# Kernel tuning notes

Hardware: AMD Instinct MI355X
Metric: run time of the kernel (lower is better)

Reference implementation:

```python
import math
import jax, jax.numpy as jnp
import numpy as np

B, S, H, NH = 2, 1536, 2048, 16
DH = H // NH  # 128
FP16_MIN = float(jnp.finfo(jnp.float16).min)


def setup_inputs() -> dict:
    key = jax.random.key(0)
    ks = jax.random.split(key, 6)
    std = 0.02
    return {
        "x": jax.random.normal(ks[0], (B, S, H), dtype=jnp.float32),
        "attention_bias": jax.random.normal(ks[1], (B, NH, S, S), dtype=jnp.float32),
        "Wq": jax.random.normal(ks[2], (H, H), dtype=jnp.float32) * std,
        "Wk": jax.random.normal(ks[3], (H, H), dtype=jnp.float32) * std,
        "Wv": jax.random.normal(ks[4], (H, H), dtype=jnp.float32) * std,
        "Wo": jax.random.normal(ks[5], (H, H), dtype=jnp.float32) * std,
    }


def reference(x, attention_bias, Wq, Wk, Wv, Wo):
    b, s, h = x.shape
    # QKV projections (nn.Linear with bias=False: y = x @ W.T)
    q = (x @ Wq.T).reshape(b, s, NH, DH).transpose(0, 2, 1, 3)  # b h s d
    k = (x @ Wk.T).reshape(b, s, NH, DH).transpose(0, 2, 1, 3)
    v = (x @ Wv.T).reshape(b, s, NH, DH).transpose(0, 2, 1, 3)
    # bias[:, :, -s:, -s:] is identity here since bias is already [b,h,s,s]
    bias = attention_bias[:, :, -s:, -s:]
    # mask where tril(bias) == 0 (upper triangle and any exact zeros in lower)
    masked = jnp.tril(bias) == 0
    bias = jnp.where(masked, FP16_MIN, bias)
    # torch SDPA default scale = 1/sqrt(head_dim) (module's softmax_scale unused)
    scale = 1.0 / math.sqrt(DH)
    scores = jnp.einsum("bhqd,bhkd->bhqk", q, k) * scale + bias
    attn = jax.nn.softmax(scores, axis=-1)
    out = jnp.einsum("bhqk,bhkd->bhqd", attn, v)  # b h s d
    out = out.transpose(0, 2, 1, 3).reshape(b, s, h)  # b s (h d)
    return out @ Wo.T
```

## Files before the change

### kernel.cpp

```cpp
#include <hip/hip_runtime.h>
#include <cstdint>
#include <stddef.h>

typedef short short8 __attribute__((ext_vector_type(8)));
typedef float floatx4 __attribute__((ext_vector_type(4)));
typedef unsigned short ushortx4 __attribute__((ext_vector_type(4)));

#define MFMA16(a, b, c) __builtin_amdgcn_mfma_f32_16x16x32_bf16((a), (b), (c), 0, 0, 0)

static constexpr int Bv = 2, Sv = 1536, Hv = 2048, NHv = 16, DHv = 128;
static constexpr int Mv = Bv * Sv;
static constexpr float SCALE = 0.08838834764831845f;

__device__ inline unsigned short f2bf(float f) {
  union { float f; unsigned u; } c; c.f = f;
  unsigned u = c.u;
  u += 0x7fffu + ((u >> 16) & 1u);
  return (unsigned short)(u >> 16);
}

__device__ inline void async_copy16(const void* g, void* l) {
  auto gp = reinterpret_cast<__attribute__((address_space(1))) uint32_t*>(
      reinterpret_cast<uintptr_t>(g));
  auto lp = reinterpret_cast<__attribute__((address_space(3))) uint32_t*>(
      reinterpret_cast<uintptr_t>(l));
  __builtin_amdgcn_global_load_lds(gp, lp, 16, 0, 0);
}

__global__ void cvt_all_kernel(const float* __restrict__ x,
    const float* __restrict__ Wq, const float* __restrict__ Wk,
    const float* __restrict__ Wv, const float* __restrict__ Wo,
    unsigned short* __restrict__ xb, unsigned short* __restrict__ wqb,
    unsigned short* __restrict__ wkb, unsigned short* __restrict__ wvb,
    unsigned short* __restrict__ wob) {
  const int i = blockIdx.x * 256 + threadIdx.x;
  const int nx4 = (Mv * Hv) / 4;
  const float* src; unsigned short* dst; int j; float scl = 1.0f;
  if (i < nx4) {
    src = x; dst = xb; j = i;
  } else {
    const int i2 = i - nx4;
    const int wsel = i2 >> 20;
    j = i2 & ((1 << 20) - 1);
    if (wsel == 0)      { src = Wq; dst = wqb; scl = SCALE; }
    else if (wsel == 1) { src = Wk; dst = wkb; }
    else if (wsel == 2) { src = Wv; dst = wvb; }
    else                { src = Wo; dst = wob; }
  }
  const float4 v = reinterpret_cast<const float4*>(src)[j];
  ushortx4 o;
  o[0] = f2bf(v.x * scl); o[1] = f2bf(v.y * scl);
  o[2] = f2bf(v.z * scl); o[3] = f2bf(v.w * scl);
  reinterpret_cast<ushortx4*>(dst)[j] = o;
}

__global__ __launch_bounds__(256, 2) void qkv_fused_kernel(
    const unsigned short* __restrict__ A,
    const unsigned short* __restrict__ Wq, const unsigned short* __restrict__ Wk,
    const unsigned short* __restrict__ Wv,
    unsigned short* __restrict__ Cq, unsigned short* __restrict__ Ck,
    unsigned short* __restrict__ Cv) {
  __shared__ __align__(16) unsigned short As[128 * 64];
  __shared__ __align__(16) unsigned short Bs[3][128 * 64];
  const int tid = threadIdx.x;
  const int w = tid >> 6, lane = tid & 63;
  const int quad = lane >> 4, l15 = lane & 15;
  const int wr = w >> 1, wc = w & 1;
  const int tileM = blockIdx.y * 128, tileN = blockIdx.x * 128;

  floatx4 aq[4][4], ak[4][4], av[4][4];
#pragma unroll
  for (int i = 0; i < 4; ++i)
#pragma unroll
    for (int j = 0; j < 4; ++j)
#pragma unroll
      for (int r = 0; r < 4; ++r) { aq[i][j][r] = 0.0f; ak[i][j][r] = 0.0f; av[i][j][r] = 0.0f; }

  size_t aoff[4], boff[4]; int lbs[4];
#pragma unroll
  for (int m = 0; m < 4; ++m) {
    const int slot = m * 256 + tid;
    const int row = slot >> 3, blk = slot & 7;
    const int sw = (blk ^ (row & 7)) * 8;
    aoff[m] = (size_t)(tileM + row) * 2048 + sw;
    boff[m] = (size_t)(tileN + row) * 2048 + sw;
    lbs[m] = (m * 256 + w * 64) * 8;
  }

  for (int k0 = 0; k0 < 2048; k0 += 64) {
    __syncthreads();
#pragma unroll
    for (int m = 0; m < 4; ++m) async_copy16(A + aoff[m] + k0, As + lbs[m]);
#pragma unroll
    for (int m = 0; m < 4; ++m) async_copy16(Wq + boff[m] + k0, Bs[0] + lbs[m]);
#pragma unroll
    for (int m = 0; m < 4; ++m) async_copy16(Wk + boff[m] + k0, Bs[1] + lbs[m]);
#pragma unroll
    for (int m = 0; m < 4; ++m) async_copy16(Wv + boff[m] + k0, Bs[2] + lbs[m]);
    __syncthreads();
#pragma unroll
    for (int kk = 0; kk < 2; ++kk) {
      const int swz = (((kk * 4 + quad) ^ (l15 & 7)) * 8);
      short8 af[4];
#pragma unroll
      for (int i = 0; i < 4; ++i)
        af[i] = *(const short8*)(As + (wr * 64 + i * 16 + l15) * 64 + swz);
      {
        short8 bq[4];
#pragma unroll
        for (int j = 0; j < 4; ++j)
          bq[j] = *(const short8*)(Bs[0] + (wc * 64 + j * 16 + l15) * 64 + swz);
#pragma unroll
        for (int i = 0; i < 4; ++i)
#pragma unroll
          for (int j = 0; j < 4; ++j) aq[i][j] = MFMA16(af[i], bq[j], aq[i][j]);
      }
      {
        short8 bk[4];
#pragma unroll
        for (int j = 0; j < 4; ++j)
          bk[j] = *(const short8*)(Bs[1] + (wc * 64 + j * 16 + l15) * 64 + swz);
#pragma unroll
        for (int i = 0; i < 4; ++i)
#pragma unroll
          for (int j = 0; j < 4; ++j) ak[i][j] = MFMA16(af[i], bk[j], ak[i][j]);
      }
      {
        short8 bv[4];
#pragma unroll
        for (int j = 0; j < 4; ++j)
          bv[j] = *(const short8*)(Bs[2] + (wc * 64 + j * 16 + l15) * 64 + swz);
#pragma unroll
        for (int i = 0; i < 4; ++i)
#pragma unroll
          for (int j = 0; j < 4; ++j) av[i][j] = MFMA16(af[i], bv[j], av[i][j]);
      }
    }
  }

#pragma unroll
  for (int i = 0; i < 4; ++i) {
#pragma unroll
    for (int r = 0; r < 4; ++r) {
      const size_t row = tileM + wr * 64 + i * 16 + quad * 4 + r;
#pragma unroll
      for (int j = 0; j < 4; ++j) {
        const int col = tileN + wc * 64 + j * 16 + l15;
        Cq[row * 2048 + col] = f2bf(aq[i][j][r]);
        Ck[row * 2048 + col] = f2bf(ak[i][j][r]);
        Cv[row * 2048 + col] = f2bf(av[i][j][r]);
      }
    }
  }
}

template <int TM, bool WF32>
__global__ __launch_bounds__(256) void gemm_bt_kernel(
    const unsigned short* __restrict__ A,
    const unsigned short* __restrict__ W0,
    void* __restrict__ C0) {
  constexpr int MI = TM / 32;
  __shared__ __align__(16) unsigned short As[2][TM * 64];
  __shared__ __align__(16) unsigned short Bs[2][128 * 64];
  const unsigned short* W = W0;
  const int tid = threadIdx.x;
  const int w = tid >> 6, lane = tid & 63;
  const int quad = lane >> 4, l15 = lane & 15;
  const int wr = w >> 1, wc = w & 1;
  const int tileM = blockIdx.y * TM, tileN = blockIdx.x * 128;

  floatx4 acc[MI][4];
#pragma unroll
  for (int i = 0; i < MI; ++i)
#pragma unroll
    for (int j = 0; j < 4; ++j)
#pragma unroll
      for (int r = 0; r < 4; ++r) acc[i][j][r] = 0.0f;

  size_t aoff[MI]; int alb[MI];
#pragma unroll
  for (int m = 0; m < MI; ++m) {
    const int slot = m * 256 + tid;
    const int row = slot >> 3, blk = slot & 7;
    aoff[m] = (size_t)(tileM + row) * 2048 + ((blk ^ (row & 7)) * 8);
    alb[m] = (m * 256 + w * 64) * 8;
  }
  size_t boff[4]; int blb[4];
#pragma unroll
  for (int m = 0; m < 4; ++m) {
    const int slot = m * 256 + tid;
    const int row = slot >> 3, blk = slot & 7;
    boff[m] = (size_t)(tileN + row) * 2048 + ((blk ^ (row & 7)) * 8);
    blb[m] = (m * 256 + w * 64) * 8;
  }

#pragma unroll
  for (int m = 0; m < MI; ++m) async_copy16(A + aoff[m], As[0] + alb[m]);
#pragma unroll
  for (int m = 0; m < 4; ++m) async_copy16(W + boff[m], Bs[0] + blb[m]);
  __syncthreads();

  for (int t = 0; t < 32; ++t) {
    const int cur = t & 1;
    if (t < 31) {
      const int kn = (t + 1) * 64;
#pragma unroll
      for (int m = 0; m < MI; ++m)
        async_copy16(A + aoff[m] + kn, As[cur ^ 1] + alb[m]);
#pragma unroll
      for (int m = 0; m < 4; ++m)
        async_copy16(W + boff[m] + kn, Bs[cur ^ 1] + blb[m]);
    }
    const unsigned short* as_ = As[cur];
    const unsigned short* bs_ = Bs[cur];
#pragma unroll
    for (int kk = 0; kk < 2; ++kk) {
      const int swz = (((kk * 4 + quad) ^ (l15 & 7)) * 8);
      short8 af[MI], bfr[4];
#pragma unroll
      for (int i = 0; i < MI; ++i)
        af[i] = *(const short8*)(as_ + (wr * (TM / 2) + i * 16 + l15) * 64 + swz);
#pragma unroll
      for (int j = 0; j < 4; ++j)
        bfr[j] = *(const short8*)(bs_ + (wc * 64 + j * 16 + l15) * 64 + swz);
#pragma unroll
      for (int i = 0; i < MI; ++i)
#pragma unroll
        for (int j = 0; j < 4; ++j) acc[i][j] = MFMA16(af[i], bfr[j], acc[i][j]);
    }
    __syncthreads();
  }

  void* C = C0;
#pragma unroll
  for (int i = 0; i < MI; ++i) {
#pragma unroll
    for (int r = 0; r < 4; ++r) {
      const int row = tileM + wr * (TM / 2) + i * 16 + quad * 4 + r;
#pragma unroll
      for (int j = 0; j < 4; ++j) {
        const int col = tileN + wc * 64 + j * 16 + l15;
        if (WF32)
          ((float*)C)[(size_t)row * 2048 + col] = acc[i][j][r];
        else
          ((unsigned short*)C)[(size_t)row * 2048 + col] = f2bf(acc[i][j][r]);
      }
    }
  }
}

__global__ __launch_bounds__(256) void vtrans_kernel(
    const unsigned short* __restrict__ V, unsigned short* __restrict__ Vtg) {
  __shared__ unsigned short Vs[64 * 132];
  const int t0 = blockIdx.x * 64, h = blockIdx.y, b = blockIdx.z;
  const int tid = threadIdx.x;
  const int w = tid >> 6, lane = tid & 63;
#pragma unroll
  for (int m = 0; m < 4; ++m) {
    const int idx = m * 256 + tid;
    const int tr = idx >> 4, blk = idx & 15;
    const unsigned short* src = V + ((size_t)(b * Sv) + t0 + tr) * Hv + h * DHv + blk * 8;
    ushortx4 v0 = *(const ushortx4*)(src);
    ushortx4 v1 = *(const ushortx4*)(src + 4);
    *(ushortx4*)(Vs + tr * 132 + blk * 8) = v0;
    *(ushortx4*)(Vs + tr * 132 + blk * 8 + 4) = v1;
  }
  __syncthreads();
  const size_t obase = ((size_t)(b * NHv + h) * DHv) * Sv + t0;
#pragma unroll 4
  for (int p = 0; p < 32; ++p) {
    const int d = p * 4 + w;
    Vtg[obase + (size_t)d * Sv + lane] = Vs[lane * 132 + d];
  }
}

__global__ __launch_bounds__(256) void attn_kernel(
    const unsigned short* __restrict__ Qg, const unsigned short* __restrict__ Kg,
    const unsigned short* __restrict__ Vtg, const float* __restrict__ bias,
    unsigned short* __restrict__ Og) {
  __shared__ __align__(16) unsigned short Ks[2][64 * 128];
  __shared__ __align__(16) unsigned short Vt[2][128 * 64];
  __shared__ __align__(16) unsigned short Ps[4 * 16 * 64];

  const int xb = blockIdx.x;
  const int qt = (xb & 1) ? (23 - (xb >> 1)) : (xb >> 1);
  const int h = blockIdx.y, b = blockIdx.z;
  const int q0 = qt * 64;
  const int tid = threadIdx.x;
  const int w = tid >> 6, lane = tid & 63;
  const int quad = lane >> 4, l15 = lane & 15;

  const size_t bh_base = (size_t)(b * Sv) * Hv + (size_t)h * DHv;
  const size_t vt_base = ((size_t)(b * NHv + h) * DHv) * Sv;

  short8 qf[4];
  {
    const unsigned short* qbase = Qg + bh_base + (size_t)(q0 + w * 16 + l15) * Hv;
#pragma unroll
    for (int kk = 0; kk < 4; ++kk)
      qf[kk] = *(const short8*)(qbase + kk * 32 + quad * 8);
  }

  floatx4 o[8];
#pragma unroll
  for (int n = 0; n < 8; ++n)
#pragma unroll
    for (int r = 0; r < 4; ++r) o[n][r] = 0.0f;
  float lrow[4] = {0.0f, 0.0f, 0.0f, 0.0f};

  const float* biasbase = bias + (size_t)(b * NHv + h) * Sv * Sv;
  unsigned short* pw = Ps + w * 1024;

  size_t koff[4], voff[4]; int lbs[4];
#pragma unroll
  for (int m = 0; m < 4; ++m) {
    const int sK = m * 256 + tid;
    const int rK = sK >> 4, bK = sK & 15;
    koff[m] = bh_base + (size_t)rK * Hv + ((bK ^ (rK & 15)) * 8);
    const int sV = m * 256 + tid;
    const int rV = sV >> 3, bV = sV & 7;
    voff[m] = vt_base + (size_t)rV * Sv + ((bV ^ (rV & 7)) * 8);
    lbs[m] = (m * 256 + w * 64) * 8;
  }

  float bv[4][4];
#pragma unroll
  for (int r = 0; r < 4; ++r) {
    const size_t brow = (size_t)(q0 + w * 16 + quad * 4 + r) * Sv;
#pragma unroll
    for (int j = 0; j < 4; ++j) bv[r][j] = biasbase[brow + j * 16 + l15];
  }

#pragma unroll
  for (int m = 0; m < 4; ++m) {
    async_copy16(Kg + koff[m], Ks[0] + lbs[m]);
    async_copy16(Vtg + voff[m], Vt[0] + lbs[m]);
  }
  __syncthreads();

  for (int kt = 0; kt <= qt; ++kt) {
    const int k0 = kt * 64;
    const int cur = kt & 1;

    if (kt < qt) {
      const int k1 = k0 + 64;
#pragma unroll
      for (int m = 0; m < 4; ++m) {
        async_copy16(Kg + koff[m] + (size_t)k1 * Hv, Ks[cur ^ 1] + lbs[m]);
        async_copy16(Vtg + voff[m] + k1, Vt[cur ^ 1] + lbs[m]);
      }
    }

    const int kn = (kt < qt) ? k0 + 64 : k0;
    float bvn[4][4];
#pragma unroll
    for (int r = 0; r < 4; ++r) {
      const size_t brow = (size_t)(q0 + w * 16 + quad * 4 + r) * Sv;
#pragma unroll
      for (int j = 0; j < 4; ++j) bvn[r][j] = biasbase[brow + kn + j * 16 + l15];
    }

    const unsigned short* ks_ = Ks[cur];
    const unsigned short* vt_ = Vt[cur];
    floatx4 sacc[4];
    __builtin_amdgcn_s_setprio(1);
#pragma unroll
    for (int j = 0; j < 4; ++j) {
#pragma unroll
      for (int r = 0; r < 4; ++r) sacc[j][r] = 0.0f;
      const int kr = j * 16 + l15;
#pragma unroll
      for (int kk = 0; kk < 4; ++kk) {
        const int g = kk * 4 + quad;
        short8 bfrag = *(const short8*)(ks_ + kr * 128 + (g ^ (kr & 15)) * 8);
        sacc[j] = MFMA16(qf[kk], bfrag, sacc[j]);
      }
    }
    __builtin_amdgcn_s_setprio(0);

    const bool diag = (kt == qt);
#pragma unroll
    for (int r = 0; r < 4; ++r) {
      const int qrow = q0 + w * 16 + quad * 4 + r;
      const int prow = quad * 4 + r;
      float acc_l = 0.0f;
#pragma unroll
      for (int j = 0; j < 4; ++j) {
        const int col = j * 16 + l15;
        float p = __expf(sacc[j][r] + bv[r][j]);
        if (diag && (k0 + col) > qrow) p = 0.0f;
        acc_l += p;
        pw[prow * 64 + ((col >> 3) ^ (prow & 7)) * 8 + (col & 7)] = f2bf(p);
      }
      lrow[r] += acc_l;
    }
#pragma unroll
    for (int r = 0; r < 4; ++r)
#pragma unroll
      for (int j = 0; j < 4; ++j) bv[r][j] = bvn[r][j];

    __builtin_amdgcn_s_setprio(1);
#pragma unroll
    for (int kk = 0; kk < 2; ++kk) {
      const int g = kk * 4 + quad;
      short8 pa = *(const short8*)(pw + l15 * 64 + (g ^ (l15 & 7)) * 8);
#pragma unroll
      for (int n = 0; n < 8; ++n) {
        const int dr = n * 16 + l15;
        short8 vbf = *(const short8*)(vt_ + dr * 64 + (g ^ (dr & 7)) * 8);
        o[n] = MFMA16(pa, vbf, o[n]);
      }
    }
    __builtin_amdgcn_s_setprio(0);

    __syncthreads();
  }

#pragma unroll
  for (int r = 0; r < 4; ++r) {
    float ls = lrow[r];
#pragma unroll
    for (int off = 1; off < 16; off <<= 1) ls += __shfl_xor(ls, off, 64);
    const float inv = 1.0f / ls;
    const int qrow = q0 + w * 16 + quad * 4 + r;
    const size_t rowbase = bh_base + (size_t)qrow * Hv;
#pragma unroll
    for (int n = 0; n < 8; ++n)
      Og[rowbase + n * 16 + l15] = f2bf(o[n][r] * inv);
  }
}

extern "C" void kernel_launch(void* const* d_in, const int* in_sizes, int n_in,
                              void* d_out, int out_size, void* d_ws, size_t ws_size,
                              hipStream_t stream) {
  const float* x = (const float*)d_in[0];
  const float* bias = (const float*)d_in[1];
  const float* Wq = (const float*)d_in[2];
  const float* Wk = (const float*)d_in[3];
  const float* Wv = (const float*)d_in[4];
  const float* Wo = (const float*)d_in[5];
  float* out = (float*)d_out;

  unsigned short* xb = (unsigned short*)d_ws;
  unsigned short* wqb = xb + (size_t)Mv * Hv;
  unsigned short* wkb = wqb + (size_t)Hv * Hv;
  unsigned short* wvb = wkb + (size_t)Hv * Hv;
  unsigned short* wob = wvb + (size_t)Hv * Hv;
  unsigned short* qb = wob + (size_t)Hv * Hv;
  unsigned short* kb = qb + (size_t)Mv * Hv;
  unsigned short* vb = kb + (size_t)Mv * Hv;
  unsigned short* ob = vb + (size_t)Mv * Hv;
  unsigned short* vtb = xb;
  const size_t needed = ((size_t)Mv * Hv * 5 + (size_t)Hv * Hv * 4) * 2;
  if (ws_size < needed) return;

  const int cvt_n = (Mv * Hv) / 4 + Hv * Hv;
  cvt_all_kernel<<<dim3(cvt_n / 256), 256, 0, stream>>>(
      x, Wq, Wk, Wv, Wo, xb, wqb, wkb, wvb, wob);

  qkv_fused_kernel<<<dim3(16, 24), 256, 0, stream>>>(
      xb, wqb, wkb, wvb, qb, kb, vb);

  vtrans_kernel<<<dim3(24, 16, 2), 256, 0, stream>>>(vb, vtb);

  attn_kernel<<<dim3(24, NHv, Bv), 256, 0, stream>>>(qb, kb, vtb, bias, ob);

  gemm_bt_kernel<128, true><<<dim3(16, 24), 256, 0, stream>>>(ob, wob, out);
}
```

Measured before the change: 613.2 us.

## Process two 64-row query tiles per attention block to reuse K/V tiles

Each attention workgroup now handles 128 query rows, split into two 64-row groups. Both groups share each staged K/V tile in LDS, which halves K/V global traffic, and the grid shrinks from 24 to 12 query blocks. Launch bounds are set to request two blocks per CU. The cost is doubled accumulator registers and fewer blocks (384), which may lower occupancy and load balance across CUs.

```diff
diff --git a/kernel.cpp b/kernel.cpp
--- a/kernel.cpp
+++ b/kernel.cpp
@@ -274,7 +274,7 @@
   }
 }
 
-__global__ __launch_bounds__(256) void attn_kernel(
+__global__ __launch_bounds__(256, 2) void attn_kernel(
     const unsigned short* __restrict__ Qg, const unsigned short* __restrict__ Kg,
     const unsigned short* __restrict__ Vtg, const float* __restrict__ bias,
     unsigned short* __restrict__ Og) {
@@ -283,9 +283,9 @@
   __shared__ __align__(16) unsigned short Ps[4 * 16 * 64];
 
   const int xb = blockIdx.x;
-  const int qt = (xb & 1) ? (23 - (xb >> 1)) : (xb >> 1);
+  const int qt = (xb & 1) ? (11 - (xb >> 1)) : (xb >> 1);
   const int h = blockIdx.y, b = blockIdx.z;
-  const int q0 = qt * 64;
+  const int q0 = qt * 128;
   const int tid = threadIdx.x;
   const int w = tid >> 6, lane = tid & 63;
   const int quad = lane >> 4, l15 = lane & 15;
@@ -293,20 +293,24 @@
   const size_t bh_base = (size_t)(b * Sv) * Hv + (size_t)h * DHv;
   const size_t vt_base = ((size_t)(b * NHv + h) * DHv) * Sv;
 
-  short8 qf[4];
-  {
-    const unsigned short* qbase = Qg + bh_base + (size_t)(q0 + w * 16 + l15) * Hv;
+  short8 qf[2][4];
+#pragma unroll
+  for (int g = 0; g < 2; ++g) {
+    const unsigned short* qbase =
+        Qg + bh_base + (size_t)(q0 + g * 64 + w * 16 + l15) * Hv;
 #pragma unroll
     for (int kk = 0; kk < 4; ++kk)
-      qf[kk] = *(const short8*)(qbase + kk * 32 + quad * 8);
-  }
-
-  floatx4 o[8];
-#pragma unroll
-  for (int n = 0; n < 8; ++n)
-#pragma unroll
-    for (int r = 0; r < 4; ++r) o[n][r] = 0.0f;
-  float lrow[4] = {0.0f, 0.0f, 0.0f, 0.0f};
+      qf[g][kk] = *(const short8*)(qbase + kk * 32 + quad * 8);
+  }
+
+  floatx4 o[2][8];
+#pragma unroll
+  for (int g = 0; g < 2; ++g)
+#pragma unroll
+    for (int n = 0; n < 8; ++n)
+#pragma unroll
+      for (int r = 0; r < 4; ++r) o[g][n][r] = 0.0f;
+  float lrow[2][4] = {{0.0f, 0.0f, 0.0f, 0.0f}, {0.0f, 0.0f, 0.0f, 0.0f}};
 
   const float* biasbase = bias + (size_t)(b * NHv + h) * Sv * Sv;
   unsigned short* pw = Ps + w * 1024;
@@ -323,12 +327,12 @@
     lbs[m] = (m * 256 + w * 64) * 8;
   }
 
-  float bv[4][4];
+  float bv0n[4][4];
 #pragma unroll
   for (int r = 0; r < 4; ++r) {
     const size_t brow = (size_t)(q0 + w * 16 + quad * 4 + r) * Sv;
 #pragma unroll
-    for (int j = 0; j < 4; ++j) bv[r][j] = biasbase[brow + j * 16 + l15];
+    for (int j = 0; j < 4; ++j) bv0n[r][j] = biasbase[brow + j * 16 + l15];
   }
 
 #pragma unroll
@@ -338,11 +342,12 @@
   }
   __syncthreads();
 
-  for (int kt = 0; kt <= qt; ++kt) {
+  const int nkt = 2 * qt + 2;
+  for (int kt = 0; kt < nkt; ++kt) {
     const int k0 = kt * 64;
     const int cur = kt & 1;
 
-    if (kt < qt) {
+    if (kt + 1 < nkt) {
       const int k1 = k0 + 64;
 #pragma unroll
       for (int m = 0; m < 4; ++m) {
@@ -351,82 +356,98 @@
       }
     }
 
-    const int kn = (kt < qt) ? k0 + 64 : k0;
-    float bvn[4][4];
+    float bv[2][4][4];
+#pragma unroll
+    for (int r = 0; r < 4; ++r)
+#pragma unroll
+      for (int j = 0; j < 4; ++j) bv[0][r][j] = bv0n[r][j];
+#pragma unroll
+    for (int r = 0; r < 4; ++r) {
+      const size_t brow = (size_t)(q0 + 64 + w * 16 + quad * 4 + r) * Sv;
+#pragma unroll
+      for (int j = 0; j < 4; ++j) bv[1][r][j] = biasbase[brow + k0 + j * 16 + l15];
+    }
+    const int knext = (kt + 1 < nkt) ? k0 + 64 : k0;
 #pragma unroll
     for (int r = 0; r < 4; ++r) {
       const size_t brow = (size_t)(q0 + w * 16 + quad * 4 + r) * Sv;
 #pragma unroll
-      for (int j = 0; j < 4; ++j) bvn[r][j] = biasbase[brow + kn + j * 16 + l15];
+      for (int j = 0; j < 4; ++j) bv0n[r][j] = biasbase[brow + knext + j * 16 + l15];
     }
 
     const unsigned short* ks_ = Ks[cur];
     const unsigned short* vt_ = Vt[cur];
-    floatx4 sacc[4];
-    __builtin_amdgcn_s_setprio(1);
-#pragma unroll
-    for (int j = 0; j < 4; ++j) {
-#pragma unroll
-      for (int r = 0; r < 4; ++r) sacc[j][r] = 0.0f;
-      const int kr = j * 16 + l15;
-#pragma unroll
-      for (int kk = 0; kk < 4; ++kk) {
-        const int g = kk * 4 + quad;
-        short8 bfrag = *(const short8*)(ks_ + kr * 128 + (g ^ (kr & 15)) * 8);
-        sacc[j] = MFMA16(qf[kk], bfrag, sacc[j]);
-      }
-    }
-    __builtin_amdgcn_s_setprio(0);
-
-    const bool diag = (kt == qt);
+
+#pragma unroll
+    for (int g = 0; g < 2; ++g) {
+      const int rbase = q0 + g * 64;
+      if (k0 == rbase + 64) continue;
+      const bool diag = (k0 == rbase);
+
+      floatx4 sacc[4];
+      __builtin_amdgcn_s_setprio(1);
+#pragma unroll
+      for (int j = 0; j < 4; ++j) {
+#pragma unroll
+        for (int r = 0; r < 4; ++r) sacc[j][r] = 0.0f;
+        const int kr = j * 16 + l15;
+#pragma unroll
+        for (int kk = 0; kk < 4; ++kk) {
+          const int gq = kk * 4 + quad;
+          short8 bfrag = *(const short8*)(ks_ + kr * 128 + (gq ^ (kr & 15)) * 8);
+          sacc[j] = MFMA16(qf[g][kk], bfrag, sacc[j]);
+        }
+      }
+      __builtin_amdgcn_s_setprio(0);
+
+#pragma unroll
+      for (int r = 0; r < 4; ++r) {
+        const int qrow = rbase + w * 16 + quad * 4 + r;
+        const int prow = quad * 4 + r;
+        float acc_l = 0.0f;
+#pragma unroll
+        for (int j = 0; j < 4; ++j) {
+          const int col = j * 16 + l15;
+          float p = __expf(sacc[j][r] + bv[g][r][j]);
+          if (diag && (k0 + col) > qrow) p = 0.0f;
+          acc_l += p;
+          pw[prow * 64 + ((col >> 3) ^ (prow & 7)) * 8 + (col & 7)] = f2bf(p);
+        }
+        lrow[g][r] += acc_l;
+      }
+
+      __builtin_amdgcn_s_setprio(1);
+#pragma unroll
+      for (int kk = 0; kk < 2; ++kk) {
+        const int gq = kk * 4 + quad;
+        short8 pa = *(const short8*)(pw + l15 * 64 + (gq ^ (l15 & 7)) * 8);
+#pragma unroll
+        for (int n = 0; n < 8; ++n) {
+          const int dr = n * 16 + l15;
+          short8 vbf = *(const short8*)(vt_ + dr * 64 + (gq ^ (dr & 7)) * 8);
+          o[g][n] = MFMA16(pa, vbf, o[g][n]);
+        }
+      }
+      __builtin_amdgcn_s_setprio(0);
+    }
+
+    __syncthreads();
+  }
+
+#pragma unroll
+  for (int g = 0; g < 2; ++g) {
 #pragma unroll
     for (int r = 0; r < 4; ++r) {
-      const int qrow = q0 + w * 16 + quad * 4 + r;
-      const int prow = quad * 4 + r;
-      float acc_l = 0.0f;
-#pragma unroll
-      for (int j = 0; j < 4; ++j) {
-        const int col = j * 16 + l15;
-        float p = __expf(sacc[j][r] + bv[r][j]);
-        if (diag && (k0 + col) > qrow) p = 0.0f;
-        acc_l += p;
-        pw[prow * 64 + ((col >> 3) ^ (prow & 7)) * 8 + (col & 7)] = f2bf(p);
-      }
-      lrow[r] += acc_l;
-    }
-#pragma unroll
-    for (int r = 0; r < 4; ++r)
-#pragma unroll
-      for (int j = 0; j < 4; ++j) bv[r][j] = bvn[r][j];
-
-    __builtin_amdgcn_s_setprio(1);
-#pragma unroll
-    for (int kk = 0; kk < 2; ++kk) {
-      const int g = kk * 4 + quad;
-      short8 pa = *(const short8*)(pw + l15 * 64 + (g ^ (l15 & 7)) * 8);
-#pragma unroll
-      for (int n = 0; n < 8; ++n) {
-        const int dr = n * 16 + l15;
-        short8 vbf = *(const short8*)(vt_ + dr * 64 + (g ^ (dr & 7)) * 8);
-        o[n] = MFMA16(pa, vbf, o[n]);
-      }
-    }
-    __builtin_amdgcn_s_setprio(0);
-
-    __syncthreads();
-  }
-
-#pragma unroll
-  for (int r = 0; r < 4; ++r) {
-    float ls = lrow[r];
-#pragma unroll
-    for (int off = 1; off < 16; off <<= 1) ls += __shfl_xor(ls, off, 64);
-    const float inv = 1.0f / ls;
-    const int qrow = q0 + w * 16 + quad * 4 + r;
-    const size_t rowbase = bh_base + (size_t)qrow * Hv;
-#pragma unroll
-    for (int n = 0; n < 8; ++n)
-      Og[rowbase + n * 16 + l15] = f2bf(o[n][r] * inv);
+      float ls = lrow[g][r];
+#pragma unroll
+      for (int off = 1; off < 16; off <<= 1) ls += __shfl_xor(ls, off, 64);
+      const float inv = 1.0f / ls;
+      const int qrow = q0 + g * 64 + w * 16 + quad * 4 + r;
+      const size_t rowbase = bh_base + (size_t)qrow * Hv;
+#pragma unroll
+      for (int n = 0; n < 8; ++n)
+        Og[rowbase + n * 16 + l15] = f2bf(o[g][n][r] * inv);
+    }
   }
 }
 
@@ -463,7 +484,7 @@
 
   vtrans_kernel<<<dim3(24, 16, 2), 256, 0, stream>>>(vb, vtb);
 
-  attn_kernel<<<dim3(24, NHv, Bv), 256, 0, stream>>>(qb, kb, vtb, bias, ob);
+  attn_kernel<<<dim3(12, NHv, Bv), 256, 0, stream>>>(qb, kb, vtb, bias, ob);
 
   gemm_bt_kernel<128, true><<<dim3(16, 24), 256, 0, stream>>>(ob, wob, out);
 }
```

After: 629.9 us. +2.7%, slower.
